# Kernel tuning notes

Measured on AMD Instinct MI355X. Metric: run time of the kernel, lower is better.

The kernel has to match this reference:

```python
import jax, jax.numpy as jnp
import numpy as np

BN_EPS = 1e-5


def _square_distance(src, dst):
    # src: (B,N,3), dst: (B,S,3) -> (B,N,S) squared euclidean distance
    d = -2.0 * jnp.einsum('bnc,bsc->bns', src, dst)
    d += jnp.sum(src * src, -1)[:, :, None]
    d += jnp.sum(dst * dst, -1)[:, None, :]
    return d


def _bn_relu(x, gamma, beta):
    # training-mode BatchNorm1d over (B, C, N): stats over (B, N)
    mean = jnp.mean(x, axis=(0, 2), keepdims=True)
    var = jnp.var(x, axis=(0, 2), keepdims=True)  # biased, as torch uses for normalization
    xhat = (x - mean) * jax.lax.rsqrt(var + BN_EPS)
    return jax.nn.relu(xhat * gamma[None, :, None] + beta[None, :, None])


def setup_inputs() -> dict:
    key = jax.random.key(0)
    ks = jax.random.split(key, 8)
    B, N, S, C1, C2 = 4, 8192, 2048, 128, 256
    inp = {
        'xyz1': jax.random.normal(ks[0], (B, 3, N), jnp.float32),
        'xyz2': jax.random.normal(ks[1], (B, 3, S), jnp.float32),
        'points1': jax.random.normal(ks[2], (B, C1, N), jnp.float32),
        'points2': jax.random.normal(ks[3], (B, C2, S), jnp.float32),
        'w0': jax.random.normal(ks[4], (256, C1 + C2), jnp.float32) * (1.0 / np.sqrt(C1 + C2)),
        'b0': jnp.zeros((256,), jnp.float32),
        'gamma0': jnp.ones((256,), jnp.float32),
        'beta0': jnp.zeros((256,), jnp.float32),
        'w1': jax.random.normal(ks[5], (128, 256), jnp.float32) * (1.0 / np.sqrt(256)),
        'b1': jnp.zeros((128,), jnp.float32),
        'gamma1': jnp.ones((128,), jnp.float32),
        'beta1': jnp.zeros((128,), jnp.float32),
    }
    return inp


def reference(xyz1, xyz2, points1, points2, w0, b0, gamma0, beta0, w1, b1, gamma1, beta1):
    B, _, N = xyz1.shape
    S = xyz2.shape[2]
    xyz1_t = jnp.transpose(xyz1, (0, 2, 1))  # (B,N,3)
    xyz2_t = jnp.transpose(xyz2, (0, 2, 1))  # (B,S,3)
    dist = _square_distance(xyz1_t, xyz2_t)  # (B,N,S)
    neg_d3, idx = jax.lax.top_k(-dist, 3)    # 3 smallest distances
    d3 = -neg_d3                             # (B,N,3)
    dist_recip = 1.0 / (d3 + 1e-8)
    weight = dist_recip / jnp.sum(dist_recip, axis=2, keepdims=True)  # (B,N,3)
    points2_t = jnp.transpose(points2, (0, 2, 1))  # (B,S,C2)
    bidx = jnp.arange(B)[:, None, None]
    neighbor = points2_t[bidx, idx]                 # (B,N,3,C2)
    interp = jnp.sum(neighbor * weight[..., None], axis=2)  # (B,N,C2)
    interp = jnp.transpose(interp, (0, 2, 1))               # (B,C2,N)
    x = jnp.concatenate([points1, interp], axis=1)          # (B,C1+C2,N)
    x = _bn_relu(jnp.einsum('oc,bcn->bon', w0, x) + b0[None, :, None], gamma0, beta0)
    x = _bn_relu(jnp.einsum('oc,bcn->bon', w1, x) + b1[None, :, None], gamma1, beta1)
    return x
```

## Files before the change

### kernel.cpp

```cpp
#include <hip/hip_runtime.h>
#include <hip/hip_bf16.h>

#define BATCH 4
#define NPTS  8192
#define SPTS  2048
#define C1    128
#define C2    256
#define CIN   384
#define H0    256
#define H1    128

typedef __attribute__((ext_vector_type(8))) short bf16x8;
typedef __attribute__((ext_vector_type(4))) float f32x4;

__device__ __forceinline__ unsigned short f2bf(float x) {
  union { float f; unsigned u; } v; v.f = x;
  unsigned r = v.u + 0x7fff + ((v.u >> 16) & 1);
  return (unsigned short)(r >> 16);
}
__device__ __forceinline__ float bf2f(unsigned short u) {
  union { unsigned u; float f; } v; v.u = ((unsigned)u) << 16; return v.f;
}

__global__ __launch_bounds__(256) void prep_kernel(
    const float* __restrict__ p2, unsigned short* __restrict__ p2tb,
    const float* __restrict__ xyz2, float4* __restrict__ xp,
    const float* __restrict__ w0, const float* __restrict__ w1,
    unsigned short* __restrict__ Wp,
    const float* __restrict__ p1, unsigned short* __restrict__ Xp) {
  __shared__ unsigned short shmem[64 * 136];
  int bid = blockIdx.x;
  int t = threadIdx.x;

  if (bid < 512) {
    int b = bid >> 7, rem = bid & 127;
    int s0 = (rem >> 2) * 64, c0 = (rem & 3) * 64;
    const float* src = p2 + (size_t)b * C2 * SPTS;
    int ss = t & 63, cseg = t >> 6;
#pragma unroll
    for (int i = 0; i < 16; i++) {
      int cc = cseg + i * 4;
      shmem[ss * 72 + cc] = f2bf(src[(size_t)(c0 + cc) * SPTS + s0 + ss]);
    }
    __syncthreads();
    int s = t >> 2, chunk = t & 3;
    uint4 v0 = *(const uint4*)&shmem[s * 72 + chunk * 16];
    uint4 v1 = *(const uint4*)&shmem[s * 72 + chunk * 16 + 8];
    unsigned short* dst = p2tb + (size_t)b * SPTS * C2 + (size_t)(s0 + s) * C2 + c0 + chunk * 16;
    *(uint4*)dst = v0;
    *(uint4*)(dst + 8) = v1;
  } else if (bid < 1024) {
    int b2 = bid - 512;
    int b = b2 >> 7, n0 = (b2 & 127) * 64;
    int nn = t & 63, c4 = t >> 6;
#pragma unroll
    for (int i = 0; i < 32; i++) {
      int c = i * 4 + c4;
      shmem[nn * 136 + c] = f2bf(p1[((size_t)b * C1 + c) * NPTS + n0 + nn]);
    }
    __syncthreads();
    int n = t >> 2;
#pragma unroll
    for (int j = 0; j < 4; j++) {
      int ch = (t & 3) + j * 4;
      uint4 v = *(const uint4*)&shmem[n * 136 + ch * 8];
      *(uint4*)&Xp[((size_t)b * NPTS + n0 + n) * CIN + ch * 8] = v;
    }
  } else if (bid < 1056) {
    int idx = (bid - 1024) * 256 + t;
    int b = idx >> 11, s = idx & (SPTS - 1);
    const float* x2 = xyz2 + (size_t)b * 3 * SPTS;
    float x = x2[s], y = x2[SPTS + s], z = x2[2 * SPTS + s];
    xp[idx] = make_float4(x, y, z, x * x + y * y + z * z);
  } else {
    int idx = ((bid - 1056) * 256 + t) * 4;
    const float* src = (idx < H0 * CIN) ? (w0 + idx) : (w1 + (idx - H0 * CIN));
    float4 v = *(const float4*)src;
    ushort4 o;
    o.x = f2bf(v.x); o.y = f2bf(v.y); o.z = f2bf(v.z); o.w = f2bf(v.w);
    *(ushort4*)(Wp + idx) = o;
  }
}

#define INS3(d, s, e0, e1, e2, j0, j1, j2)                        \
  {                                                               \
    bool lt0 = (d) < (e0), lt1 = (d) < (e1), lt2 = (d) < (e2);    \
    j2 = lt1 ? (j1) : (lt2 ? (s) : (j2));                         \
    j1 = lt0 ? (j0) : (lt1 ? (s) : (j1));                         \
    j0 = lt0 ? (s) : (j0);                                        \
    e2 = __builtin_amdgcn_fmed3f((d), (e1), (e2));                \
    e1 = __builtin_amdgcn_fmed3f((d), (e0), (e1));                \
    e0 = fminf((d), (e0));                                        \
  }

__global__ __launch_bounds__(1024) void knn_kernel(
    const float* __restrict__ xyz1, const float4* __restrict__ xp,
    int* __restrict__ nidx, float* __restrict__ nw) {
  int b = blockIdx.y;
  int t = threadIdx.x;
  int lane = t & 63;
  int w = __builtin_amdgcn_readfirstlane(t >> 6);
  int n = blockIdx.x * 64 + lane;
  const float* x1 = xyz1 + (size_t)b * 3 * NPTS;
  float px = x1[n], py = x1[NPTS + n], pz = x1[2 * NPTS + n];

  const int CHUNK = SPTS / 16;
  int sbase = w * CHUNK;
  const float4* cp = xp + (size_t)b * SPTS + sbase;

  float d0 = 3e38f, d1 = 3e38f, d2 = 3e38f;
  int i0 = 0, i1 = 0, i2 = 0;
#pragma unroll 8
  for (int j = 0; j < CHUNK; j++) {
    float4 c = cp[j];
    float qc = fmaf(py, c.y, px * c.x);
    qc = fmaf(pz, c.z, qc);
    float d = fmaf(-2.f, qc, c.w);
    int s = sbase + j;
    INS3(d, s, d0, d1, d2, i0, i1, i2);
  }

  __shared__ float dsh[16][64][3];
  __shared__ int   ish[16][64][3];
  dsh[w][lane][0] = d0; dsh[w][lane][1] = d1; dsh[w][lane][2] = d2;
  ish[w][lane][0] = i0; ish[w][lane][1] = i1; ish[w][lane][2] = i2;
  __syncthreads();

  if (t < 256) {
    int g = t >> 6, q = t & 63;
    float e0 = 3e38f, e1 = 3e38f, e2 = 3e38f;
    int j0 = 0, j1 = 0, j2 = 0;
#pragma unroll
    for (int c = 0; c < 4; c++) {
#pragma unroll
      for (int k = 0; k < 3; k++) {
        float d = dsh[4 * g + c][q][k];
        int s = ish[4 * g + c][q][k];
        INS3(d, s, e0, e1, e2, j0, j1, j2);
      }
    }
    dsh[4 * g][q][0] = e0; dsh[4 * g][q][1] = e1; dsh[4 * g][q][2] = e2;
    ish[4 * g][q][0] = j0; ish[4 * g][q][1] = j1; ish[4 * g][q][2] = j2;
  }
  __syncthreads();

  if (t < 64) {
    float e0 = 3e38f, e1 = 3e38f, e2 = 3e38f;
    int j0 = 0, j1 = 0, j2 = 0;
#pragma unroll
    for (int c = 0; c < 4; c++) {
#pragma unroll
      for (int k = 0; k < 3; k++) {
        float d = dsh[4 * c][t][k];
        int s = ish[4 * c][t][k];
        INS3(d, s, e0, e1, e2, j0, j1, j2);
      }
    }
    float qq = px * px + py * py + pz * pz;
    float r0 = 1.f / (e0 + qq + 1e-8f);
    float r1 = 1.f / (e1 + qq + 1e-8f);
    float r2 = 1.f / (e2 + qq + 1e-8f);
    float rs = 1.f / (r0 + r1 + r2);
    int base = (b * NPTS + n) * 3;
    nidx[base + 0] = j0; nidx[base + 1] = j1; nidx[base + 2] = j2;
    nw[base + 0] = r0 * rs; nw[base + 1] = r1 * rs; nw[base + 2] = r2 * rs;
  }
}

__global__ __launch_bounds__(256) void interp_kernel(
    const unsigned short* __restrict__ p2tb, const int* __restrict__ nidx,
    const float* __restrict__ nw, unsigned short* __restrict__ Xp) {
  const int PTS = 8;
  int bid = blockIdx.x;
  int b = bid / (NPTS / PTS);
  int p0 = (bid % (NPTS / PTS)) * PTS;
  int c = threadIdx.x;
  const unsigned short* base = p2tb + (size_t)b * SPTS * C2;
#pragma unroll
  for (int k = 0; k < PTS; k++) {
    int p = p0 + k;
    int ib = (b * NPTS + p) * 3;
    int i0 = nidx[ib], i1 = nidx[ib + 1], i2 = nidx[ib + 2];
    float w0v = nw[ib], w1v = nw[ib + 1], w2v = nw[ib + 2];
    float v = w0v * bf2f(base[(size_t)i0 * C2 + c]) +
              w1v * bf2f(base[(size_t)i1 * C2 + c]) +
              w2v * bf2f(base[(size_t)i2 * C2 + c]);
    Xp[((size_t)b * NPTS + p) * CIN + C1 + c] = f2bf(v);
  }
}

template <int MT, int KD, bool OUT_BF16>
__global__ __launch_bounds__(256) void mfma_gemm_kernel(
    const unsigned short* __restrict__ A, const unsigned short* __restrict__ X,
    const float* __restrict__ bias, void* __restrict__ Yv) {
  __shared__ unsigned short As[128 * 32];
  __shared__ unsigned short Bs[128 * 32];
  int b = blockIdx.z;
  int n0 = blockIdx.x * 128;
  int o0 = blockIdx.y * 128;
  int t = threadIdx.x;
  int lane = t & 63;
  int w = __builtin_amdgcn_readfirstlane(t >> 6);
  int mhalf = (w & 1) * 64, nhalf = (w >> 1) * 64;
  const unsigned short* Xb = X + (size_t)b * NPTS * KD;

  f32x4 acc[4][4] = {};

  int rA = lane >> 2;
  int cofs = (lane & 3) * 8;

  for (int k0 = 0; k0 < KD; k0 += 32) {
#pragma unroll
    for (int q = 0; q < 2; q++) {
      int r0 = w * 32 + q * 16;
      const unsigned short* ga = A + (size_t)(o0 + r0 + rA) * KD + k0 + cofs;
      __builtin_amdgcn_global_load_lds(
          (const __attribute__((address_space(1))) void*)ga,
          (__attribute__((address_space(3))) void*)(As + r0 * 32), 16, 0, 0);
      const unsigned short* gb = Xb + (size_t)(n0 + r0 + rA) * KD + k0 + cofs;
      __builtin_amdgcn_global_load_lds(
          (const __attribute__((address_space(1))) void*)gb,
          (__attribute__((address_space(3))) void*)(Bs + r0 * 32), 16, 0, 0);
    }
    __syncthreads();

    bf16x8 af[4], bfr[4];
    int mi = lane & 15, kq = (lane >> 4) * 8;
#pragma unroll
    for (int i = 0; i < 4; i++) {
      af[i]  = *(const bf16x8*)(As + (mhalf + i * 16 + mi) * 32 + kq);
      bfr[i] = *(const bf16x8*)(Bs + (nhalf + i * 16 + mi) * 32 + kq);
    }
#pragma unroll
    for (int mt = 0; mt < 4; mt++)
#pragma unroll
      for (int nt = 0; nt < 4; nt++)
        acc[mt][nt] = __builtin_amdgcn_mfma_f32_16x16x32_bf16(
            af[mt], bfr[nt], acc[mt][nt], 0, 0, 0);
    __syncthreads();
  }

  int mi = lane & 15;
  int rq = (lane >> 4) * 4;
#pragma unroll
  for (int mt = 0; mt < 4; mt++) {
#pragma unroll
    for (int r = 0; r < 4; r++) {
      int m = o0 + mhalf + mt * 16 + rq + r;
      float bv = bias[m];
#pragma unroll
      for (int nt = 0; nt < 4; nt++) {
        int n = n0 + nhalf + nt * 16 + mi;
        float v = acc[mt][nt][r] + bv;
        if constexpr (OUT_BF16) {
          unsigned short* Y = (unsigned short*)Yv + (size_t)b * MT * NPTS;
          Y[(size_t)m * NPTS + n] = f2bf(v);
        } else {
          float* Y = (float*)Yv + (size_t)b * MT * NPTS;
          Y[(size_t)m * NPTS + n] = v;
        }
      }
    }
  }
}

template <int C>
__global__ __launch_bounds__(256) void bn_stats_bf16_kernel(
    const unsigned short* __restrict__ Y, const float* __restrict__ gamma,
    const float* __restrict__ beta, float* __restrict__ a, float* __restrict__ s) {
  int o = blockIdx.x;
  int t = threadIdx.x;
  float sum = 0.f, sq = 0.f;
  for (int b = 0; b < BATCH; b++) {
    const unsigned short* p = Y + ((size_t)b * C + o) * NPTS;
    for (int n = t * 4; n < NPTS; n += 1024) {
      ushort4 v = *(const ushort4*)(p + n);
      float x0 = bf2f(v.x), x1 = bf2f(v.y), x2 = bf2f(v.z), x3 = bf2f(v.w);
      sum += x0 + x1 + x2 + x3;
      sq += x0 * x0 + x1 * x1 + x2 * x2 + x3 * x3;
    }
  }
  __shared__ float r1[256], r2[256];
  r1[t] = sum; r2[t] = sq;
  __syncthreads();
  for (int off = 128; off > 0; off >>= 1) {
    if (t < off) { r1[t] += r1[t + off]; r2[t] += r2[t + off]; }
    __syncthreads();
  }
  if (t == 0) {
    float inv = 1.f / (float)(BATCH * NPTS);
    float mean = r1[0] * inv;
    float var = r2[0] * inv - mean * mean;
    float ia = gamma[o] * rsqrtf(var + 1e-5f);
    a[o] = ia;
    s[o] = beta[o] - mean * ia;
  }
}

template <int C>
__global__ __launch_bounds__(256) void bn_stats_kernel(
    const float* __restrict__ Y, const float* __restrict__ gamma,
    const float* __restrict__ beta, float* __restrict__ a, float* __restrict__ s) {
  int o = blockIdx.x;
  int t = threadIdx.x;
  float sum = 0.f, sq = 0.f;
  for (int b = 0; b < BATCH; b++) {
    const float* p = Y + ((size_t)b * C + o) * NPTS;
    for (int n = t * 4; n < NPTS; n += 1024) {
      float4 v = *(const float4*)(p + n);
      sum += v.x + v.y + v.z + v.w;
      sq += v.x * v.x + v.y * v.y + v.z * v.z + v.w * v.w;
    }
  }
  __shared__ float r1[256], r2[256];
  r1[t] = sum; r2[t] = sq;
  __syncthreads();
  for (int off = 128; off > 0; off >>= 1) {
    if (t < off) { r1[t] += r1[t + off]; r2[t] += r2[t + off]; }
    __syncthreads();
  }
  if (t == 0) {
    float inv = 1.f / (float)(BATCH * NPTS);
    float mean = r1[0] * inv;
    float var = r2[0] * inv - mean * mean;
    float ia = gamma[o] * rsqrtf(var + 1e-5f);
    a[o] = ia;
    s[o] = beta[o] - mean * ia;
  }
}

__global__ __launch_bounds__(256) void bn0_apply_kernel(
    const unsigned short* __restrict__ Y0, const float* __restrict__ a,
    const float* __restrict__ s, unsigned short* __restrict__ X1) {
  __shared__ unsigned short tile[64][80];
  int b = blockIdx.z, o0 = blockIdx.y * 64, n0 = blockIdx.x * 64;
  int t = threadIdx.x;
  int nn = t & 63, o4 = t >> 6;
#pragma unroll
  for (int i = 0; i < 16; i++) {
    int o = i * 4 + o4;
    float v = bf2f(Y0[((size_t)b * H0 + o0 + o) * NPTS + n0 + nn]);
    v = fmaxf(v * a[o0 + o] + s[o0 + o], 0.f);
    tile[nn][o] = f2bf(v);
  }
  __syncthreads();
  int n = t >> 2;
#pragma unroll
  for (int j = 0; j < 2; j++) {
    int ch = (t & 3) + j * 4;
    uint4 v = *(const uint4*)&tile[n][ch * 8];
    *(uint4*)&X1[((size_t)b * NPTS + n0 + n) * H0 + o0 + ch * 8] = v;
  }
}

__global__ __launch_bounds__(256) void bn_apply_kernel(
    float* __restrict__ Y, const float* __restrict__ a, const float* __restrict__ s) {
  int idx = blockIdx.x * 256 + threadIdx.x;
  int i = idx * 4;
  int c = (i >> 13) & (H1 - 1);
  float ia = a[c], sh = s[c];
  float4 v = *(float4*)(Y + i);
  v.x = fmaxf(v.x * ia + sh, 0.f);
  v.y = fmaxf(v.y * ia + sh, 0.f);
  v.z = fmaxf(v.z * ia + sh, 0.f);
  v.w = fmaxf(v.w * ia + sh, 0.f);
  *(float4*)(Y + i) = v;
}

extern "C" void kernel_launch(void* const* d_in, const int* in_sizes, int n_in,
                              void* d_out, int out_size, void* d_ws, size_t ws_size,
                              hipStream_t stream) {
  const float* xyz1    = (const float*)d_in[0];
  const float* xyz2    = (const float*)d_in[1];
  const float* points1 = (const float*)d_in[2];
  const float* points2 = (const float*)d_in[3];
  const float* w0      = (const float*)d_in[4];
  const float* b0      = (const float*)d_in[5];
  const float* gamma0  = (const float*)d_in[6];
  const float* beta0   = (const float*)d_in[7];
  const float* w1      = (const float*)d_in[8];
  const float* b1      = (const float*)d_in[9];
  const float* gamma1  = (const float*)d_in[10];
  const float* beta1   = (const float*)d_in[11];
  float* out = (float*)d_out;

  char* ws = (char*)d_ws;
  unsigned short* p2tb = (unsigned short*)ws;  ws += (size_t)BATCH * SPTS * C2 * 2;
  unsigned short* Xp = (unsigned short*)ws;    ws += (size_t)BATCH * NPTS * CIN * 2;
  unsigned short* Y0 = (unsigned short*)ws;    ws += (size_t)BATCH * H0 * NPTS * 2;
  unsigned short* X1 = (unsigned short*)ws;    ws += (size_t)BATCH * NPTS * H0 * 2;
  unsigned short* Wp = (unsigned short*)ws;    ws += (size_t)(H0 * CIN + H1 * H0) * 2;
  int* nidx = (int*)ws;                        ws += (size_t)BATCH * NPTS * 3 * 4;
  float* nw = (float*)ws;                      ws += (size_t)BATCH * NPTS * 3 * 4;
  float4* xyz2p = (float4*)(((uintptr_t)ws + 15) & ~(uintptr_t)15);
  ws = (char*)xyz2p + (size_t)BATCH * SPTS * 16;
  float* a0 = (float*)ws;                      ws += 1024;
  float* s0 = (float*)ws;                      ws += 1024;
  float* a1 = (float*)ws;                      ws += 1024;
  float* s1 = (float*)ws;                      ws += 1024;
  (void)ws_size; (void)in_sizes; (void)n_in; (void)out_size;

  prep_kernel<<<dim3(1184), 256, 0, stream>>>(points2, p2tb, xyz2, xyz2p,
                                              w0, w1, Wp, points1, Xp);
  knn_kernel<<<dim3(NPTS / 64, BATCH), 1024, 0, stream>>>(xyz1, xyz2p, nidx, nw);
  interp_kernel<<<dim3(BATCH * NPTS / 8), 256, 0, stream>>>(p2tb, nidx, nw, Xp);

  mfma_gemm_kernel<H0, CIN, true><<<dim3(NPTS / 128, H0 / 128, BATCH), 256, 0, stream>>>(
      Wp, Xp, b0, Y0);
  bn_stats_bf16_kernel<H0><<<H0, 256, 0, stream>>>(Y0, gamma0, beta0, a0, s0);
  bn0_apply_kernel<<<dim3(NPTS / 64, H0 / 64, BATCH), 256, 0, stream>>>(Y0, a0, s0, X1);
  mfma_gemm_kernel<H1, H0, false><<<dim3(NPTS / 128, H1 / 128, BATCH), 256, 0, stream>>>(
      Wp + H0 * CIN, X1, b1, out);
  bn_stats_kernel<H1><<<H1, 256, 0, stream>>>(out, gamma1, beta1, a1, s1);
  bn_apply_kernel<<<dim3(BATCH * H1 * NPTS / 1024), 256, 0, stream>>>(out, a1, s1);
}
```

Measured before the change: 197.4 us.

## Fuse interpolation into first GEMM and BN statistics into GEMM epilogues

Result: slower. 297.5 us (+50.7%).

```diff
diff --git a/kernel.cpp b/kernel.cpp
--- a/kernel.cpp
+++ b/kernel.cpp
@@ -9,6 +9,7 @@
 #define CIN   384
 #define H0    256
 #define H1    128
+#define NTOTF 32768.0f
 
 typedef __attribute__((ext_vector_type(8))) short bf16x8;
 typedef __attribute__((ext_vector_type(4))) float f32x4;
@@ -20,6 +21,15 @@
 }
 __device__ __forceinline__ float bf2f(unsigned short u) {
   union { unsigned u; float f; } v; v.u = ((unsigned)u) << 16; return v.f;
+}
+__device__ __forceinline__ float bflo(unsigned u) {
+  union { unsigned x; float f; } v; v.x = u << 16; return v.f;
+}
+__device__ __forceinline__ float bfhi(unsigned u) {
+  union { unsigned x; float f; } v; v.x = u & 0xffff0000u; return v.f;
+}
+__device__ __forceinline__ unsigned pack2(float lo, float hi) {
+  return ((unsigned)f2bf(hi) << 16) | (unsigned)f2bf(lo);
 }
 
 __global__ __launch_bounds__(256) void prep_kernel(
@@ -27,7 +37,8 @@
     const float* __restrict__ xyz2, float4* __restrict__ xp,
     const float* __restrict__ w0, const float* __restrict__ w1,
     unsigned short* __restrict__ Wp,
-    const float* __restrict__ p1, unsigned short* __restrict__ Xp) {
+    const float* __restrict__ p1, unsigned short* __restrict__ Xp,
+    float* __restrict__ gstats) {
   __shared__ unsigned short shmem[64 * 136];
   int bid = blockIdx.x;
   int t = threadIdx.x;
@@ -64,7 +75,7 @@
     for (int j = 0; j < 4; j++) {
       int ch = (t & 3) + j * 4;
       uint4 v = *(const uint4*)&shmem[n * 136 + ch * 8];
-      *(uint4*)&Xp[((size_t)b * NPTS + n0 + n) * CIN + ch * 8] = v;
+      *(uint4*)&Xp[((size_t)b * NPTS + n0 + n) * C1 + ch * 8] = v;
     }
   } else if (bid < 1056) {
     int idx = (bid - 1024) * 256 + t;
@@ -72,13 +83,16 @@
     const float* x2 = xyz2 + (size_t)b * 3 * SPTS;
     float x = x2[s], y = x2[SPTS + s], z = x2[2 * SPTS + s];
     xp[idx] = make_float4(x, y, z, x * x + y * y + z * z);
-  } else {
+  } else if (bid < 1184) {
     int idx = ((bid - 1056) * 256 + t) * 4;
     const float* src = (idx < H0 * CIN) ? (w0 + idx) : (w1 + (idx - H0 * CIN));
     float4 v = *(const float4*)src;
     ushort4 o;
     o.x = f2bf(v.x); o.y = f2bf(v.y); o.z = f2bf(v.z); o.w = f2bf(v.w);
     *(ushort4*)(Wp + idx) = o;
+  } else {
+#pragma unroll
+    for (int j = 0; j < 3; j++) gstats[t + 256 * j] = 0.f;
   }
 }
 
@@ -167,34 +181,15 @@
   }
 }
 
-__global__ __launch_bounds__(256) void interp_kernel(
+__global__ __launch_bounds__(256) void gemm1_kernel(
+    const unsigned short* __restrict__ Wp, const unsigned short* __restrict__ Xp1,
     const unsigned short* __restrict__ p2tb, const int* __restrict__ nidx,
-    const float* __restrict__ nw, unsigned short* __restrict__ Xp) {
-  const int PTS = 8;
-  int bid = blockIdx.x;
-  int b = bid / (NPTS / PTS);
-  int p0 = (bid % (NPTS / PTS)) * PTS;
-  int c = threadIdx.x;
-  const unsigned short* base = p2tb + (size_t)b * SPTS * C2;
-#pragma unroll
-  for (int k = 0; k < PTS; k++) {
-    int p = p0 + k;
-    int ib = (b * NPTS + p) * 3;
-    int i0 = nidx[ib], i1 = nidx[ib + 1], i2 = nidx[ib + 2];
-    float w0v = nw[ib], w1v = nw[ib + 1], w2v = nw[ib + 2];
-    float v = w0v * bf2f(base[(size_t)i0 * C2 + c]) +
-              w1v * bf2f(base[(size_t)i1 * C2 + c]) +
-              w2v * bf2f(base[(size_t)i2 * C2 + c]);
-    Xp[((size_t)b * NPTS + p) * CIN + C1 + c] = f2bf(v);
-  }
-}
-
-template <int MT, int KD, bool OUT_BF16>
-__global__ __launch_bounds__(256) void mfma_gemm_kernel(
-    const unsigned short* __restrict__ A, const unsigned short* __restrict__ X,
-    const float* __restrict__ bias, void* __restrict__ Yv) {
+    const float* __restrict__ nw, const float* __restrict__ bias,
+    unsigned short* __restrict__ Y0, float* __restrict__ gsum, float* __restrict__ gsq) {
   __shared__ unsigned short As[128 * 32];
   __shared__ unsigned short Bs[128 * 32];
+  __shared__ int   sIdx[128 * 3];
+  __shared__ float sW[128 * 3];
   int b = blockIdx.z;
   int n0 = blockIdx.x * 128;
   int o0 = blockIdx.y * 128;
@@ -202,25 +197,61 @@
   int lane = t & 63;
   int w = __builtin_amdgcn_readfirstlane(t >> 6);
   int mhalf = (w & 1) * 64, nhalf = (w >> 1) * 64;
-  const unsigned short* Xb = X + (size_t)b * NPTS * KD;
+
+  if (t < 128) {
+    int ib = (b * NPTS + n0 + t) * 3;
+#pragma unroll
+    for (int j = 0; j < 3; j++) { sIdx[t * 3 + j] = nidx[ib + j]; sW[t * 3 + j] = nw[ib + j]; }
+  }
+  __syncthreads();
+
+  const unsigned short* p2b = p2tb + (size_t)b * SPTS * C2;
+  const unsigned short* Xb  = Xp1 + (size_t)b * NPTS * C1;
 
   f32x4 acc[4][4] = {};
-
   int rA = lane >> 2;
   int cofs = (lane & 3) * 8;
 
-  for (int k0 = 0; k0 < KD; k0 += 32) {
+  for (int k0 = 0; k0 < CIN; k0 += 32) {
 #pragma unroll
     for (int q = 0; q < 2; q++) {
       int r0 = w * 32 + q * 16;
-      const unsigned short* ga = A + (size_t)(o0 + r0 + rA) * KD + k0 + cofs;
+      const unsigned short* ga = Wp + (size_t)(o0 + r0 + rA) * CIN + k0 + cofs;
       __builtin_amdgcn_global_load_lds(
           (const __attribute__((address_space(1))) void*)ga,
           (__attribute__((address_space(3))) void*)(As + r0 * 32), 16, 0, 0);
-      const unsigned short* gb = Xb + (size_t)(n0 + r0 + rA) * KD + k0 + cofs;
-      __builtin_amdgcn_global_load_lds(
-          (const __attribute__((address_space(1))) void*)gb,
-          (__attribute__((address_space(3))) void*)(Bs + r0 * 32), 16, 0, 0);
+    }
+    if (k0 < C1) {
+#pragma unroll
+      for (int q = 0; q < 2; q++) {
+        int r0 = w * 32 + q * 16;
+        const unsigned short* gb = Xb + (size_t)(n0 + r0 + rA) * C1 + k0 + cofs;
+        __builtin_amdgcn_global_load_lds(
+            (const __attribute__((address_space(1))) void*)gb,
+            (__attribute__((address_space(3))) void*)(Bs + r0 * 32), 16, 0, 0);
+      }
+    } else {
+      int r = w * 32 + (lane >> 1);
+      int cb = (k0 - C1) + (lane & 1) * 16;
+      int i0 = sIdx[r * 3], i1 = sIdx[r * 3 + 1], i2 = sIdx[r * 3 + 2];
+      float w0v = sW[r * 3], w1v = sW[r * 3 + 1], w2v = sW[r * 3 + 2];
+      const uint4* g0 = (const uint4*)(p2b + (size_t)i0 * C2 + cb);
+      const uint4* g1 = (const uint4*)(p2b + (size_t)i1 * C2 + cb);
+      const uint4* g2 = (const uint4*)(p2b + (size_t)i2 * C2 + cb);
+      uint4 a0 = g0[0], b0 = g0[1];
+      uint4 a1 = g1[0], b1 = g1[1];
+      uint4 a2 = g2[0], b2 = g2[1];
+#define MIX(d0, d1, d2) pack2(w0v * bflo(d0) + w1v * bflo(d1) + w2v * bflo(d2), \
+                              w0v * bfhi(d0) + w1v * bfhi(d1) + w2v * bfhi(d2))
+      uint4 o0v, o1v;
+      o0v.x = MIX(a0.x, a1.x, a2.x); o0v.y = MIX(a0.y, a1.y, a2.y);
+      o0v.z = MIX(a0.z, a1.z, a2.z); o0v.w = MIX(a0.w, a1.w, a2.w);
+      o1v.x = MIX(b0.x, b1.x, b2.x); o1v.y = MIX(b0.y, b1.y, b2.y);
+      o1v.z = MIX(b0.z, b1.z, b2.z); o1v.w = MIX(b0.w, b1.w, b2.w);
+#undef MIX
+      uint4* dst = (uint4*)&Bs[r * 32 + (lane & 1) * 16];
+      dst[0] = o0v;
+      dst[1] = o1v;
     }
     __syncthreads();
 
@@ -242,105 +273,50 @@
 
   int mi = lane & 15;
   int rq = (lane >> 4) * 4;
+  unsigned short* Yb = Y0 + (size_t)b * H0 * NPTS;
 #pragma unroll
   for (int mt = 0; mt < 4; mt++) {
 #pragma unroll
     for (int r = 0; r < 4; r++) {
       int m = o0 + mhalf + mt * 16 + rq + r;
       float bv = bias[m];
+      float sv = 0.f, sq = 0.f;
 #pragma unroll
       for (int nt = 0; nt < 4; nt++) {
         int n = n0 + nhalf + nt * 16 + mi;
         float v = acc[mt][nt][r] + bv;
-        if constexpr (OUT_BF16) {
-          unsigned short* Y = (unsigned short*)Yv + (size_t)b * MT * NPTS;
-          Y[(size_t)m * NPTS + n] = f2bf(v);
-        } else {
-          float* Y = (float*)Yv + (size_t)b * MT * NPTS;
-          Y[(size_t)m * NPTS + n] = v;
-        }
-      }
-    }
-  }
-}
-
-template <int C>
-__global__ __launch_bounds__(256) void bn_stats_bf16_kernel(
-    const unsigned short* __restrict__ Y, const float* __restrict__ gamma,
-    const float* __restrict__ beta, float* __restrict__ a, float* __restrict__ s) {
-  int o = blockIdx.x;
-  int t = threadIdx.x;
-  float sum = 0.f, sq = 0.f;
-  for (int b = 0; b < BATCH; b++) {
-    const unsigned short* p = Y + ((size_t)b * C + o) * NPTS;
-    for (int n = t * 4; n < NPTS; n += 1024) {
-      ushort4 v = *(const ushort4*)(p + n);
-      float x0 = bf2f(v.x), x1 = bf2f(v.y), x2 = bf2f(v.z), x3 = bf2f(v.w);
-      sum += x0 + x1 + x2 + x3;
-      sq += x0 * x0 + x1 * x1 + x2 * x2 + x3 * x3;
-    }
-  }
-  __shared__ float r1[256], r2[256];
-  r1[t] = sum; r2[t] = sq;
-  __syncthreads();
-  for (int off = 128; off > 0; off >>= 1) {
-    if (t < off) { r1[t] += r1[t + off]; r2[t] += r2[t + off]; }
-    __syncthreads();
-  }
-  if (t == 0) {
-    float inv = 1.f / (float)(BATCH * NPTS);
-    float mean = r1[0] * inv;
-    float var = r2[0] * inv - mean * mean;
-    float ia = gamma[o] * rsqrtf(var + 1e-5f);
-    a[o] = ia;
-    s[o] = beta[o] - mean * ia;
-  }
-}
-
-template <int C>
-__global__ __launch_bounds__(256) void bn_stats_kernel(
-    const float* __restrict__ Y, const float* __restrict__ gamma,
-    const float* __restrict__ beta, float* __restrict__ a, float* __restrict__ s) {
-  int o = blockIdx.x;
-  int t = threadIdx.x;
-  float sum = 0.f, sq = 0.f;
-  for (int b = 0; b < BATCH; b++) {
-    const float* p = Y + ((size_t)b * C + o) * NPTS;
-    for (int n = t * 4; n < NPTS; n += 1024) {
-      float4 v = *(const float4*)(p + n);
-      sum += v.x + v.y + v.z + v.w;
-      sq += v.x * v.x + v.y * v.y + v.z * v.z + v.w * v.w;
-    }
-  }
-  __shared__ float r1[256], r2[256];
-  r1[t] = sum; r2[t] = sq;
-  __syncthreads();
-  for (int off = 128; off > 0; off >>= 1) {
-    if (t < off) { r1[t] += r1[t + off]; r2[t] += r2[t + off]; }
-    __syncthreads();
-  }
-  if (t == 0) {
-    float inv = 1.f / (float)(BATCH * NPTS);
-    float mean = r1[0] * inv;
-    float var = r2[0] * inv - mean * mean;
-    float ia = gamma[o] * rsqrtf(var + 1e-5f);
-    a[o] = ia;
-    s[o] = beta[o] - mean * ia;
+        Yb[(size_t)m * NPTS + n] = f2bf(v);
+        sv += v; sq += v * v;
+      }
+#pragma unroll
+      for (int msk = 1; msk < 16; msk <<= 1) {
+        sv += __shfl_xor(sv, msk);
+        sq += __shfl_xor(sq, msk);
+      }
+      if (mi == 0) { atomicAdd(&gsum[m], sv); atomicAdd(&gsq[m], sq); }
+    }
   }
 }
 
 __global__ __launch_bounds__(256) void bn0_apply_kernel(
-    const unsigned short* __restrict__ Y0, const float* __restrict__ a,
-    const float* __restrict__ s, unsigned short* __restrict__ X1) {
+    const unsigned short* __restrict__ Y0, const float* __restrict__ gsum,
+    const float* __restrict__ gsq, const float* __restrict__ gamma,
+    const float* __restrict__ beta, unsigned short* __restrict__ X1) {
   __shared__ unsigned short tile[64][80];
   int b = blockIdx.z, o0 = blockIdx.y * 64, n0 = blockIdx.x * 64;
   int t = threadIdx.x;
   int nn = t & 63, o4 = t >> 6;
+  const float inv = 1.f / NTOTF;
 #pragma unroll
   for (int i = 0; i < 16; i++) {
     int o = i * 4 + o4;
-    float v = bf2f(Y0[((size_t)b * H0 + o0 + o) * NPTS + n0 + nn]);
-    v = fmaxf(v * a[o0 + o] + s[o0 + o], 0.f);
+    int oc = o0 + o;
+    float mean = gsum[oc] * inv;
+    float var = gsq[oc] * inv - mean * mean;
+    float ia = gamma[oc] * rsqrtf(var + 1e-5f);
+    float sh = beta[oc] - mean * ia;
+    float v = bf2f(Y0[((size_t)b * H0 + oc) * NPTS + n0 + nn]);
+    v = fmaxf(v * ia + sh, 0.f);
     tile[nn][o] = f2bf(v);
   }
   __syncthreads();
@@ -353,12 +329,93 @@
   }
 }
 
+__global__ __launch_bounds__(256) void gemm2_kernel(
+    const unsigned short* __restrict__ A, const unsigned short* __restrict__ X,
+    const float* __restrict__ bias, float* __restrict__ Y,
+    float* __restrict__ gsum, float* __restrict__ gsq) {
+  __shared__ unsigned short As[128 * 32];
+  __shared__ unsigned short Bs[128 * 32];
+  int b = blockIdx.z;
+  int n0 = blockIdx.x * 128;
+  int t = threadIdx.x;
+  int lane = t & 63;
+  int w = __builtin_amdgcn_readfirstlane(t >> 6);
+  int mhalf = (w & 1) * 64, nhalf = (w >> 1) * 64;
+  const unsigned short* Xb = X + (size_t)b * NPTS * H0;
+
+  f32x4 acc[4][4] = {};
+  int rA = lane >> 2;
+  int cofs = (lane & 3) * 8;
+
+  for (int k0 = 0; k0 < H0; k0 += 32) {
+#pragma unroll
+    for (int q = 0; q < 2; q++) {
+      int r0 = w * 32 + q * 16;
+      const unsigned short* ga = A + (size_t)(r0 + rA) * H0 + k0 + cofs;
+      __builtin_amdgcn_global_load_lds(
+          (const __attribute__((address_space(1))) void*)ga,
+          (__attribute__((address_space(3))) void*)(As + r0 * 32), 16, 0, 0);
+      const unsigned short* gb = Xb + (size_t)(n0 + r0 + rA) * H0 + k0 + cofs;
+      __builtin_amdgcn_global_load_lds(
+          (const __attribute__((address_space(1))) void*)gb,
+          (__attribute__((address_space(3))) void*)(Bs + r0 * 32), 16, 0, 0);
+    }
+    __syncthreads();
+
+    bf16x8 af[4], bfr[4];
+    int mi = lane & 15, kq = (lane >> 4) * 8;
+#pragma unroll
+    for (int i = 0; i < 4; i++) {
+      af[i]  = *(const bf16x8*)(As + (mhalf + i * 16 + mi) * 32 + kq);
+      bfr[i] = *(const bf16x8*)(Bs + (nhalf + i * 16 + mi) * 32 + kq);
+    }
+#pragma unroll
+    for (int mt = 0; mt < 4; mt++)
+#pragma unroll
+      for (int nt = 0; nt < 4; nt++)
+        acc[mt][nt] = __builtin_amdgcn_mfma_f32_16x16x32_bf16(
+            af[mt], bfr[nt], acc[mt][nt], 0, 0, 0);
+    __syncthreads();
+  }
+
+  int mi = lane & 15;
+  int rq = (lane >> 4) * 4;
+  float* Yb = Y + (size_t)b * H1 * NPTS;
+#pragma unroll
+  for (int mt = 0; mt < 4; mt++) {
+#pragma unroll
+    for (int r = 0; r < 4; r++) {
+      int m = mhalf + mt * 16 + rq + r;
+      float bv = bias[m];
+      float sv = 0.f, sq = 0.f;
+#pragma unroll
+      for (int nt = 0; nt < 4; nt++) {
+        int n = n0 + nhalf + nt * 16 + mi;
+        float v = acc[mt][nt][r] + bv;
+        Yb[(size_t)m * NPTS + n] = v;
+        sv += v; sq += v * v;
+      }
+#pragma unroll
+      for (int msk = 1; msk < 16; msk <<= 1) {
+        sv += __shfl_xor(sv, msk);
+        sq += __shfl_xor(sq, msk);
+      }
+      if (mi == 0) { atomicAdd(&gsum[m], sv); atomicAdd(&gsq[m], sq); }
+    }
+  }
+}
+
 __global__ __launch_bounds__(256) void bn_apply_kernel(
-    float* __restrict__ Y, const float* __restrict__ a, const float* __restrict__ s) {
+    float* __restrict__ Y, const float* __restrict__ gsum, const float* __restrict__ gsq,
+    const float* __restrict__ gamma, const float* __restrict__ beta) {
   int idx = blockIdx.x * 256 + threadIdx.x;
   int i = idx * 4;
   int c = (i >> 13) & (H1 - 1);
-  float ia = a[c], sh = s[c];
+  const float inv = 1.f / NTOTF;
+  float mean = gsum[c] * inv;
+  float var = gsq[c] * inv - mean * mean;
+  float ia = gamma[c] * rsqrtf(var + 1e-5f);
+  float sh = beta[c] - mean * ia;
   float4 v = *(float4*)(Y + i);
   v.x = fmaxf(v.x * ia + sh, 0.f);
   v.y = fmaxf(v.y * ia + sh, 0.f);
@@ -386,7 +443,7 @@
 
   char* ws = (char*)d_ws;
   unsigned short* p2tb = (unsigned short*)ws;  ws += (size_t)BATCH * SPTS * C2 * 2;
-  unsigned short* Xp = (unsigned short*)ws;    ws += (size_t)BATCH * NPTS * CIN * 2;
+  unsigned short* Xp = (unsigned short*)ws;    ws += (size_t)BATCH * NPTS * C1 * 2;
   unsigned short* Y0 = (unsigned short*)ws;    ws += (size_t)BATCH * H0 * NPTS * 2;
   unsigned short* X1 = (unsigned short*)ws;    ws += (size_t)BATCH * NPTS * H0 * 2;
   unsigned short* Wp = (unsigned short*)ws;    ws += (size_t)(H0 * CIN + H1 * H0) * 2;
@@ -394,23 +451,22 @@
   float* nw = (float*)ws;                      ws += (size_t)BATCH * NPTS * 3 * 4;
   float4* xyz2p = (float4*)(((uintptr_t)ws + 15) & ~(uintptr_t)15);
   ws = (char*)xyz2p + (size_t)BATCH * SPTS * 16;
-  float* a0 = (float*)ws;                      ws += 1024;
-  float* s0 = (float*)ws;                      ws += 1024;
-  float* a1 = (float*)ws;                      ws += 1024;
-  float* s1 = (float*)ws;                      ws += 1024;
+  float* gstats = (float*)ws;                  ws += 768 * 4;
+  float* gsum0 = gstats;
+  float* gsq0  = gstats + 256;
+  float* gsum1 = gstats + 512;
+  float* gsq1  = gstats + 640;
   (void)ws_size; (void)in_sizes; (void)n_in; (void)out_size;
 
-  prep_kernel<<<dim3(1184), 256, 0, stream>>>(points2, p2tb, xyz2, xyz2p,
-                                              w0, w1, Wp, points1, Xp);
+  prep_kernel<<<dim3(1185), 256, 0, stream>>>(points2, p2tb, xyz2, xyz2p,
+                                              w0, w1, Wp, points1, Xp, gstats);
   knn_kernel<<<dim3(NPTS / 64, BATCH), 1024, 0, stream>>>(xyz1, xyz2p, nidx, nw);
-  interp_kernel<<<dim3(BATCH * NPTS / 8), 256, 0, stream>>>(p2tb, nidx, nw, Xp);
-
-  mfma_gemm_kernel<H0, CIN, true><<<dim3(NPTS / 128, H0 / 128, BATCH), 256, 0, stream>>>(
-      Wp, Xp, b0, Y0);
-  bn_stats_bf16_kernel<H0><<<H0, 256, 0, stream>>>(Y0, gamma0, beta0, a0, s0);
-  bn0_apply_kernel<<<dim3(NPTS / 64, H0 / 64, BATCH), 256, 0, stream>>>(Y0, a0, s0, X1);
-  mfma_gemm_kernel<H1, H0, false><<<dim3(NPTS / 128, H1 / 128, BATCH), 256, 0, stream>>>(
-      Wp + H0 * CIN, X1, b1, out);
-  bn_stats_kernel<H1><<<H1, 256, 0, stream>>>(out, gamma1, beta1, a1, s1);
-  bn_apply_kernel<<<dim3(BATCH * H1 * NPTS / 1024), 256, 0, stream>>>(out, a1, s1);
-}
+  gemm1_kernel<<<dim3(NPTS / 128, H0 / 128, BATCH), 256, 0, stream>>>(
+      Wp, Xp, p2tb, nidx, nw, b0, Y0, gsum0, gsq0);
+  bn0_apply_kernel<<<dim3(NPTS / 64, H0 / 64, BATCH), 256, 0, stream>>>(
+      Y0, gsum0, gsq0, gamma0, beta0, X1);
+  gemm2_kernel<<<dim3(NPTS / 128, 1, BATCH), 256, 0, stream>>>(
+      Wp + H0 * CIN, X1, b1, out, gsum1, gsq1);
+  bn_apply_kernel<<<dim3(BATCH * H1 * NPTS / 1024), 256, 0, stream>>>(
+      out, gsum1, gsq1, gamma1, beta1);
+}
```

## Fuse BatchNorm statistics into GEMM epilogue via atomics, drop stats kernels

Applied to the files above, without the earlier changes.

Result: slower. 317.0 us (+60.6%).

```diff
diff --git a/kernel.cpp b/kernel.cpp
--- a/kernel.cpp
+++ b/kernel.cpp
@@ -9,6 +9,7 @@
 #define CIN   384
 #define H0    256
 #define H1    128
+#define NTOTF 32768.0f
 
 typedef __attribute__((ext_vector_type(8))) short bf16x8;
 typedef __attribute__((ext_vector_type(4))) float f32x4;
@@ -27,7 +28,8 @@
     const float* __restrict__ xyz2, float4* __restrict__ xp,
     const float* __restrict__ w0, const float* __restrict__ w1,
     unsigned short* __restrict__ Wp,
-    const float* __restrict__ p1, unsigned short* __restrict__ Xp) {
+    const float* __restrict__ p1, unsigned short* __restrict__ Xp,
+    float* __restrict__ gstats) {
   __shared__ unsigned short shmem[64 * 136];
   int bid = blockIdx.x;
   int t = threadIdx.x;
@@ -72,13 +74,16 @@
     const float* x2 = xyz2 + (size_t)b * 3 * SPTS;
     float x = x2[s], y = x2[SPTS + s], z = x2[2 * SPTS + s];
     xp[idx] = make_float4(x, y, z, x * x + y * y + z * z);
-  } else {
+  } else if (bid < 1184) {
     int idx = ((bid - 1056) * 256 + t) * 4;
     const float* src = (idx < H0 * CIN) ? (w0 + idx) : (w1 + (idx - H0 * CIN));
     float4 v = *(const float4*)src;
     ushort4 o;
     o.x = f2bf(v.x); o.y = f2bf(v.y); o.z = f2bf(v.z); o.w = f2bf(v.w);
     *(ushort4*)(Wp + idx) = o;
+  } else {
+#pragma unroll
+    for (int j = 0; j < 3; j++) gstats[t + 256 * j] = 0.f;
   }
 }
 
@@ -192,7 +197,8 @@
 template <int MT, int KD, bool OUT_BF16>
 __global__ __launch_bounds__(256) void mfma_gemm_kernel(
     const unsigned short* __restrict__ A, const unsigned short* __restrict__ X,
-    const float* __restrict__ bias, void* __restrict__ Yv) {
+    const float* __restrict__ bias, void* __restrict__ Yv,
+    float* __restrict__ gsum, float* __restrict__ gsq) {
   __shared__ unsigned short As[128 * 32];
   __shared__ unsigned short Bs[128 * 32];
   int b = blockIdx.z;
@@ -205,7 +211,6 @@
   const unsigned short* Xb = X + (size_t)b * NPTS * KD;
 
   f32x4 acc[4][4] = {};
-
   int rA = lane >> 2;
   int cofs = (lane & 3) * 8;
 
@@ -248,6 +253,7 @@
     for (int r = 0; r < 4; r++) {
       int m = o0 + mhalf + mt * 16 + rq + r;
       float bv = bias[m];
+      float sv = 0.f, sq = 0.f;
 #pragma unroll
       for (int nt = 0; nt < 4; nt++) {
         int n = n0 + nhalf + nt * 16 + mi;
@@ -259,88 +265,37 @@
           float* Y = (float*)Yv + (size_t)b * MT * NPTS;
           Y[(size_t)m * NPTS + n] = v;
         }
+        sv += v; sq += v * v;
       }
-    }
-  }
-}
-
-template <int C>
-__global__ __launch_bounds__(256) void bn_stats_bf16_kernel(
-    const unsigned short* __restrict__ Y, const float* __restrict__ gamma,
-    const float* __restrict__ beta, float* __restrict__ a, float* __restrict__ s) {
-  int o = blockIdx.x;
-  int t = threadIdx.x;
-  float sum = 0.f, sq = 0.f;
-  for (int b = 0; b < BATCH; b++) {
-    const unsigned short* p = Y + ((size_t)b * C + o) * NPTS;
-    for (int n = t * 4; n < NPTS; n += 1024) {
-      ushort4 v = *(const ushort4*)(p + n);
-      float x0 = bf2f(v.x), x1 = bf2f(v.y), x2 = bf2f(v.z), x3 = bf2f(v.w);
-      sum += x0 + x1 + x2 + x3;
-      sq += x0 * x0 + x1 * x1 + x2 * x2 + x3 * x3;
-    }
-  }
-  __shared__ float r1[256], r2[256];
-  r1[t] = sum; r2[t] = sq;
-  __syncthreads();
-  for (int off = 128; off > 0; off >>= 1) {
-    if (t < off) { r1[t] += r1[t + off]; r2[t] += r2[t + off]; }
-    __syncthreads();
-  }
-  if (t == 0) {
-    float inv = 1.f / (float)(BATCH * NPTS);
-    float mean = r1[0] * inv;
-    float var = r2[0] * inv - mean * mean;
-    float ia = gamma[o] * rsqrtf(var + 1e-5f);
-    a[o] = ia;
-    s[o] = beta[o] - mean * ia;
-  }
-}
-
-template <int C>
-__global__ __launch_bounds__(256) void bn_stats_kernel(
-    const float* __restrict__ Y, const float* __restrict__ gamma,
-    const float* __restrict__ beta, float* __restrict__ a, float* __restrict__ s) {
-  int o = blockIdx.x;
-  int t = threadIdx.x;
-  float sum = 0.f, sq = 0.f;
-  for (int b = 0; b < BATCH; b++) {
-    const float* p = Y + ((size_t)b * C + o) * NPTS;
-    for (int n = t * 4; n < NPTS; n += 1024) {
-      float4 v = *(const float4*)(p + n);
-      sum += v.x + v.y + v.z + v.w;
-      sq += v.x * v.x + v.y * v.y + v.z * v.z + v.w * v.w;
-    }
-  }
-  __shared__ float r1[256], r2[256];
-  r1[t] = sum; r2[t] = sq;
-  __syncthreads();
-  for (int off = 128; off > 0; off >>= 1) {
-    if (t < off) { r1[t] += r1[t + off]; r2[t] += r2[t + off]; }
-    __syncthreads();
-  }
-  if (t == 0) {
-    float inv = 1.f / (float)(BATCH * NPTS);
-    float mean = r1[0] * inv;
-    float var = r2[0] * inv - mean * mean;
-    float ia = gamma[o] * rsqrtf(var + 1e-5f);
-    a[o] = ia;
-    s[o] = beta[o] - mean * ia;
+#pragma unroll
+      for (int msk = 1; msk < 16; msk <<= 1) {
+        sv += __shfl_xor(sv, msk);
+        sq += __shfl_xor(sq, msk);
+      }
+      if (mi == 0) { atomicAdd(&gsum[m], sv); atomicAdd(&gsq[m], sq); }
+    }
   }
 }
 
 __global__ __launch_bounds__(256) void bn0_apply_kernel(
-    const unsigned short* __restrict__ Y0, const float* __restrict__ a,
-    const float* __restrict__ s, unsigned short* __restrict__ X1) {
+    const unsigned short* __restrict__ Y0, const float* __restrict__ gsum,
+    const float* __restrict__ gsq, const float* __restrict__ gamma,
+    const float* __restrict__ beta, unsigned short* __restrict__ X1) {
   __shared__ unsigned short tile[64][80];
   int b = blockIdx.z, o0 = blockIdx.y * 64, n0 = blockIdx.x * 64;
   int t = threadIdx.x;
   int nn = t & 63, o4 = t >> 6;
+  const float inv = 1.f / NTOTF;
 #pragma unroll
   for (int i = 0; i < 16; i++) {
     int o = i * 4 + o4;
-    float v = bf2f(Y0[((size_t)b * H0 + o0 + o) * NPTS + n0 + nn]);
-    v = fmaxf(v * a[o0 + o] + s[o0 + o], 0.f);
+    int oc = o0 + o;
+    float mean = gsum[oc] * inv;
+    float var = gsq[oc] * inv - mean * mean;
+    float ia = gamma[oc] * rsqrtf(var + 1e-5f);
+    float sh = beta[oc] - mean * ia;
+    float v = bf2f(Y0[((size_t)b * H0 + oc) * NPTS + n0 + nn]);
+    v = fmaxf(v * ia + sh, 0.f);
     tile[nn][o] = f2bf(v);
   }
   __syncthreads();
@@ -354,11 +309,16 @@
 }
 
 __global__ __launch_bounds__(256) void bn_apply_kernel(
-    float* __restrict__ Y, const float* __restrict__ a, const float* __restrict__ s) {
+    float* __restrict__ Y, const float* __restrict__ gsum, const float* __restrict__ gsq,
+    const float* __restrict__ gamma, const float* __restrict__ beta) {
   int idx = blockIdx.x * 256 + threadIdx.x;
   int i = idx * 4;
   int c = (i >> 13) & (H1 - 1);
-  float ia = a[c], sh = s[c];
+  const float inv = 1.f / NTOTF;
+  float mean = gsum[c] * inv;
+  float var = gsq[c] * inv - mean * mean;
+  float ia = gamma[c] * rsqrtf(var + 1e-5f);
+  float sh = beta[c] - mean * ia;
   float4 v = *(float4*)(Y + i);
   v.x = fmaxf(v.x * ia + sh, 0.f);
   v.y = fmaxf(v.y * ia + sh, 0.f);
@@ -394,23 +354,24 @@
   float* nw = (float*)ws;                      ws += (size_t)BATCH * NPTS * 3 * 4;
   float4* xyz2p = (float4*)(((uintptr_t)ws + 15) & ~(uintptr_t)15);
   ws = (char*)xyz2p + (size_t)BATCH * SPTS * 16;
-  float* a0 = (float*)ws;                      ws += 1024;
-  float* s0 = (float*)ws;                      ws += 1024;
-  float* a1 = (float*)ws;                      ws += 1024;
-  float* s1 = (float*)ws;                      ws += 1024;
+  float* gstats = (float*)ws;                  ws += 768 * 4;
+  float* gsum0 = gstats;
+  float* gsq0  = gstats + 256;
+  float* gsum1 = gstats + 512;
+  float* gsq1  = gstats + 640;
   (void)ws_size; (void)in_sizes; (void)n_in; (void)out_size;
 
-  prep_kernel<<<dim3(1184), 256, 0, stream>>>(points2, p2tb, xyz2, xyz2p,
-                                              w0, w1, Wp, points1, Xp);
+  prep_kernel<<<dim3(1185), 256, 0, stream>>>(points2, p2tb, xyz2, xyz2p,
+                                              w0, w1, Wp, points1, Xp, gstats);
   knn_kernel<<<dim3(NPTS / 64, BATCH), 1024, 0, stream>>>(xyz1, xyz2p, nidx, nw);
   interp_kernel<<<dim3(BATCH * NPTS / 8), 256, 0, stream>>>(p2tb, nidx, nw, Xp);
 
   mfma_gemm_kernel<H0, CIN, true><<<dim3(NPTS / 128, H0 / 128, BATCH), 256, 0, stream>>>(
-      Wp, Xp, b0, Y0);
-  bn_stats_bf16_kernel<H0><<<H0, 256, 0, stream>>>(Y0, gamma0, beta0, a0, s0);
-  bn0_apply_kernel<<<dim3(NPTS / 64, H0 / 64, BATCH), 256, 0, stream>>>(Y0, a0, s0, X1);
-  mfma_gemm_kernel<H1, H0, false><<<dim3(NPTS / 128, H1 / 128, BATCH), 256, 0, stream>>>(
-      Wp + H0 * CIN, X1, b1, out);
-  bn_stats_kernel<H1><<<H1, 256, 0, stream>>>(out, gamma1, beta1, a1, s1);
-  bn_apply_kernel<<<dim3(BATCH * H1 * NPTS / 1024), 256, 0, stream>>>(out, a1, s1);
-}
+      Wp, Xp, b0, Y0, gsum0, gsq0);
+  bn0_apply_kernel<<<dim3(NPTS / 64, H0 / 64, BATCH), 256, 0, stream>>>(
+      Y0, gsum0, gsq0, gamma0, beta0, X1);
+  mfma_gemm_kernel<H1, H0, false><<<dim3(NPTS / 128, 1, BATCH), 256, 0, stream>>>(
+      Wp + H0 * CIN, X1, b1, out, gsum1, gsq1);
+  bn_apply_kernel<<<dim3(BATCH * H1 * NPTS / 1024), 256, 0, stream>>>(
+      out, gsum1, gsq1, gamma1, beta1);
+}
```
